# Performance work log

Measured on AMD Instinct MI355X. Metric: run time of the kernel, lower is better.

The kernel has to match this reference:

```python
import jax, jax.numpy as jnp
import numpy as np

CONNECTION_STRENGTH = 3.0   # hardcoded in AMN.forward
DIRECT_WEIGHT = 1.5         # direct_weight_initial
CONN_THRESHOLD = 0.1


def setup_inputs() -> dict:
    key = jax.random.key(0)
    k1, k2, k3, k4, k5 = jax.random.split(key, 5)
    U, T, N = 128, 256, 1024
    return {
        "input_spikes": (jax.random.uniform(k1, (T, N)) < 0.1).astype(jnp.float32),
        "unit_outputs": jax.random.uniform(k2, (U, T, N), dtype=jnp.float32),  # stacked ModularUnit outputs
        "conn": jax.random.uniform(k3, (U, U), dtype=jnp.float32),             # sampled connection matrix
        "target_spikes": (jax.random.uniform(k4, (T, N)) < 0.3).astype(jnp.float32),  # encode_number output
        "rand_bias": jax.random.uniform(k5, (T, N), dtype=jnp.float32),        # torch.rand_like for boost
    }


def reference(input_spikes, unit_outputs, conn, target_spikes, rand_bias):
    # get_spike_rate: mean firing rate in Hz (spikes.mean() * 1000)
    input_rate = input_spikes.mean() * 1000.0
    target_rate = input_rate + 20.0

    # Fused threshold-gated weighted aggregation:
    # for i,j: if conn[i,j] > 0.1: final += unit_outputs[j] * conn[i,j] * 3.0
    gated = jnp.where(conn > CONN_THRESHOLD, conn, 0.0)           # [U,U]
    w = CONNECTION_STRENGTH * gated.sum(axis=0)                   # [U] total inbound weight per source j
    final = jnp.einsum('j,jtn->tn', w, unit_outputs)              # [T,N]

    # Direct mapping heuristic
    final = final * 0.5 + target_spikes * DIRECT_WEIGHT

    # Conditional boost when mean activity is low
    mean = final.mean()
    target_mean = target_rate / 100.0
    boost = jnp.maximum(0.0, target_mean - mean)
    final = jnp.where(mean < 0.2, final + rand_bias * boost * 2.0, final)
    return final
```

## Files before the change

### kernel.cpp

```cpp
#include <hip/hip_runtime.h>

#define U   128
#define T_  256
#define N_  1024
#define TN  (T_ * N_)


__global__ __launch_bounds__(1024) void prep_kernel(const float* __restrict__ conn,
                                                    float* __restrict__ ws) {
    __shared__ float part[8][U];
    int tid = threadIdx.x;
    int c = tid >> 7;
    int j = tid & 127;
    float s = 0.0f;
#pragma unroll
    for (int k = 0; k < 16; ++k) {
        float v = conn[(c * 16 + k) * U + j];
        s += (v > 0.1f) ? v : 0.0f;
    }
    part[c][j] = s;
    __syncthreads();
    if (tid < 2) ws[tid] = 0.0f;
    if (tid < U) {
        float t = 0.0f;
#pragma unroll
        for (int cc = 0; cc < 8; ++cc) t += part[cc][tid];
        ws[2 + tid] = 3.0f * t;
    }
}

__global__ __launch_bounds__(256) void main_kernel(const float* __restrict__ uo,
                                                   const float* __restrict__ tgt,
                                                   const float* __restrict__ insp,
                                                   float* __restrict__ out,
                                                   float* __restrict__ ws) {
    __shared__ float w_s[U];
    int tid = threadIdx.x;
    if (tid < U) w_s[tid] = ws[2 + tid];
    __syncthreads();

    int idx = blockIdx.x * 256 + tid;
    const float* p = uo + idx;

    float acc = 0.0f;
#pragma unroll 16
    for (int j = 0; j < U; ++j)
        acc += w_s[j] * __builtin_nontemporal_load(p + (size_t)j * TN);

    float r = acc * 0.5f + 1.5f * tgt[idx];
    out[idx] = r;
    float lin = insp[idx];

#pragma unroll
    for (int off = 32; off > 0; off >>= 1) {
        r   += __shfl_down(r,   off, 64);
        lin += __shfl_down(lin, off, 64);
    }
    __shared__ float red[8];
    int wave = tid >> 6;
    int lane = tid & 63;
    if (lane == 0) { red[wave] = r; red[4 + wave] = lin; }
    __syncthreads();
    if (tid == 0) {
        atomicAdd(&ws[0], red[0] + red[1] + red[2] + red[3]);
        atomicAdd(&ws[1], red[4] + red[5] + red[6] + red[7]);
    }
}

__global__ __launch_bounds__(256) void boost_kernel(const float4* __restrict__ rb,
                                                    float4* __restrict__ out,
                                                    const float* __restrict__ ws) {
    float mean    = ws[0] * (1.0f / TN);
    float in_rate = ws[1] * (1000.0f / TN);
    float target_mean = (in_rate + 20.0f) * 0.01f;
    float boost = fmaxf(0.0f, target_mean - mean);
    if (mean < 0.2f) {
        int idx = blockIdx.x * 256 + threadIdx.x;
        float4 o = out[idx];
        float4 r = rb[idx];
        float b2 = boost * 2.0f;
        o.x += r.x * b2;
        o.y += r.y * b2;
        o.z += r.z * b2;
        o.w += r.w * b2;
        out[idx] = o;
    }
}

extern "C" void kernel_launch(void* const* d_in, const int* in_sizes, int n_in,
                              void* d_out, int out_size, void* d_ws, size_t ws_size,
                              hipStream_t stream) {
    const float* input_spikes = (const float*)d_in[0];
    const float* unit_outputs = (const float*)d_in[1];
    const float* conn         = (const float*)d_in[2];
    const float* target       = (const float*)d_in[3];
    const float* rand_bias    = (const float*)d_in[4];
    float* out = (float*)d_out;
    float* ws  = (float*)d_ws;

    prep_kernel<<<1, 1024, 0, stream>>>(conn, ws);

    main_kernel<<<TN / 256, 256, 0, stream>>>(
        unit_outputs, target, input_spikes, out, ws);

    boost_kernel<<<(TN / 4) / 256, 256, 0, stream>>>(
        (const float4*)rand_bias, (float4*)out, ws);
}
```

Measured before the change: 214.2 us.

## Split unit reduction across groups with vectorized prefetched loads and combine pass

Splits the 128-unit weighted reduction into 8 groups of 16 units, each handled by separate blocks over 64 tiles. Threads use float4 nontemporal loads with a one-step software prefetch, and write per-group partial sums to workspace. A new combine kernel sums the partials, applies the target term and does the mean reductions. This aims to raise memory-level parallelism and load width on the 128 MB streaming read. In exchange it adds an 8 MB partial-sum write and read-back, plus an extra kernel launch, and it assumes the workspace is large enough.

Result: faster. 204.6 us (-4.4%).

```diff
diff --git a/kernel.cpp b/kernel.cpp
--- a/kernel.cpp
+++ b/kernel.cpp
@@ -1,9 +1,14 @@
 #include <hip/hip_runtime.h>
 
-#define U   128
-#define T_  256
-#define N_  1024
-#define TN  (T_ * N_)
+#define U     128
+#define TN    (256 * 1024)
+#define TN4   (TN / 4)
+#define GJ    8
+#define JPG   (U / GJ)
+#define TILES 64
+#define TILE_F4 (TN4 / TILES)
+
+typedef float vfloat4 __attribute__((ext_vector_type(4)));
 
 
 __global__ __launch_bounds__(1024) void prep_kernel(const float* __restrict__ conn,
@@ -29,46 +34,84 @@
     }
 }
 
-__global__ __launch_bounds__(256) void main_kernel(const float* __restrict__ uo,
-                                                   const float* __restrict__ tgt,
-                                                   const float* __restrict__ insp,
-                                                   float* __restrict__ out,
+__global__ __launch_bounds__(256) void main_kernel(const vfloat4* __restrict__ uo,
                                                    float* __restrict__ ws) {
-    __shared__ float w_s[U];
-    int tid = threadIdx.x;
-    if (tid < U) w_s[tid] = ws[2 + tid];
-    __syncthreads();
+    int tile = blockIdx.x & (TILES - 1);
+    int g    = blockIdx.x / TILES;
+    int tid  = threadIdx.x;
 
-    int idx = blockIdx.x * 256 + tid;
-    const float* p = uo + idx;
+    const float* wp = ws + 2 + g * JPG;
+    vfloat4* part = (vfloat4*)(ws + 256) + (size_t)g * TN4;
 
-    float acc = 0.0f;
-#pragma unroll 16
-    for (int j = 0; j < U; ++j)
-        acc += w_s[j] * __builtin_nontemporal_load(p + (size_t)j * TN);
+    size_t base = (size_t)tile * TILE_F4 + tid;
+    const vfloat4* pu = uo + (size_t)(g * JPG) * TN4 + base;
 
-    float r = acc * 0.5f + 1.5f * tgt[idx];
+    vfloat4 acc0 = 0.0f, acc1 = 0.0f, acc2 = 0.0f, acc3 = 0.0f;
+
+    vfloat4 b0 = __builtin_nontemporal_load(pu + 0);
+    vfloat4 b1 = __builtin_nontemporal_load(pu + 256);
+    vfloat4 b2 = __builtin_nontemporal_load(pu + 512);
+    vfloat4 b3 = __builtin_nontemporal_load(pu + 768);
+
+    for (int jj = 0; jj < JPG; ++jj) {
+        float wj = wp[jj];
+        vfloat4 c0 = b0, c1 = b1, c2 = b2, c3 = b3;
+        if (jj + 1 < JPG) {
+            const vfloat4* pn = pu + (size_t)(jj + 1) * TN4;
+            b0 = __builtin_nontemporal_load(pn + 0);
+            b1 = __builtin_nontemporal_load(pn + 256);
+            b2 = __builtin_nontemporal_load(pn + 512);
+            b3 = __builtin_nontemporal_load(pn + 768);
+        }
+        acc0 += wj * c0;
+        acc1 += wj * c1;
+        acc2 += wj * c2;
+        acc3 += wj * c3;
+    }
+
+    part[base + 0]   = acc0;
+    part[base + 256] = acc1;
+    part[base + 512] = acc2;
+    part[base + 768] = acc3;
+}
+
+__global__ __launch_bounds__(256) void combine_kernel(const vfloat4* __restrict__ tgt,
+                                                      const vfloat4* __restrict__ insp,
+                                                      vfloat4* __restrict__ out,
+                                                      float* __restrict__ ws) {
+    int idx = blockIdx.x * 256 + threadIdx.x;
+    const vfloat4* part = (const vfloat4*)(ws + 256);
+
+    vfloat4 s = part[idx];
+#pragma unroll
+    for (int g = 1; g < GJ; ++g)
+        s += part[(size_t)g * TN4 + idx];
+
+    vfloat4 t = tgt[idx];
+    vfloat4 r = s * 0.5f + 1.5f * t;
     out[idx] = r;
-    float lin = insp[idx];
 
+    vfloat4 is = insp[idx];
+    float lsum = r.x + r.y + r.z + r.w;
+    float lin  = is.x + is.y + is.z + is.w;
 #pragma unroll
     for (int off = 32; off > 0; off >>= 1) {
-        r   += __shfl_down(r,   off, 64);
-        lin += __shfl_down(lin, off, 64);
+        lsum += __shfl_down(lsum, off, 64);
+        lin  += __shfl_down(lin,  off, 64);
     }
     __shared__ float red[8];
-    int wave = tid >> 6;
-    int lane = tid & 63;
-    if (lane == 0) { red[wave] = r; red[4 + wave] = lin; }
+    int wave = threadIdx.x >> 6;
+    int lane = threadIdx.x & 63;
+    if (lane == 0) { red[wave] = lsum; red[4 + wave] = lin; }
     __syncthreads();
-    if (tid == 0) {
+    if (threadIdx.x == 0) {
         atomicAdd(&ws[0], red[0] + red[1] + red[2] + red[3]);
         atomicAdd(&ws[1], red[4] + red[5] + red[6] + red[7]);
     }
 }
 
-__global__ __launch_bounds__(256) void boost_kernel(const float4* __restrict__ rb,
-                                                    float4* __restrict__ out,
+__global__ __launch_bounds__(256) void boost_kernel(const vfloat4* __restrict__ rb,
+                                                    vfloat4* __restrict__ out,
                                                     const float* __restrict__ ws) {
     float mean    = ws[0] * (1.0f / TN);
     float in_rate = ws[1] * (1000.0f / TN);
@@ -76,14 +119,9 @@
     float boost = fmaxf(0.0f, target_mean - mean);
     if (mean < 0.2f) {
         int idx = blockIdx.x * 256 + threadIdx.x;
-        float4 o = out[idx];
-        float4 r = rb[idx];
-        float b2 = boost * 2.0f;
-        o.x += r.x * b2;
-        o.y += r.y * b2;
-        o.z += r.z * b2;
-        o.w += r.w * b2;
-        out[idx] = o;
+        vfloat4 o = out[idx];
+        vfloat4 r = rb[idx];
+        out[idx] = o + r * (boost * 2.0f);
     }
 }
 
@@ -100,9 +138,12 @@
 
     prep_kernel<<<1, 1024, 0, stream>>>(conn, ws);
 
-    main_kernel<<<TN / 256, 256, 0, stream>>>(
-        unit_outputs, target, input_spikes, out, ws);
+    main_kernel<<<TILES * GJ, 256, 0, stream>>>(
+        (const vfloat4*)unit_outputs, ws);
 
-    boost_kernel<<<(TN / 4) / 256, 256, 0, stream>>>(
-        (const float4*)rand_bias, (float4*)out, ws);
+    combine_kernel<<<TN4 / 256, 256, 0, stream>>>(
+        (const vfloat4*)target, (const vfloat4*)input_spikes, (vfloat4*)out, ws);
+
+    boost_kernel<<<TN4 / 256, 256, 0, stream>>>(
+        (const vfloat4*)rand_bias, (vfloat4*)out, ws);
 }
```

## Fuse conn prep into main kernel, vectorize loads, replace atomics with per-block partials

Applied to the files above, without the earlier changes.

The gate-and-sum over conn now runs redundantly in every block of the main kernel, which removes the separate single-block prep launch. The main kernel loads float4 vectors, so it runs only 256 blocks with four outputs per thread. Per-block partial sums go to workspace slots instead of atomics, and the boost kernel reduces these 256 partials in each block before applying the boost. The risk is fewer blocks in flight for a bandwidth-bound 128 MB stream, plus the redundant conn reads per block.

After: 192.8 us. -10.0%, faster.

```diff
diff --git a/kernel.cpp b/kernel.cpp
--- a/kernel.cpp
+++ b/kernel.cpp
@@ -1,89 +1,95 @@
 #include <hip/hip_runtime.h>
 
-#define U   128
-#define T_  256
-#define N_  1024
-#define TN  (T_ * N_)
+#define U    128
+#define TN   (256 * 1024)
+#define TN4  (TN / 4)
+#define NBLK 256
+
+typedef float vfloat4 __attribute__((ext_vector_type(4)));
 
 
-__global__ __launch_bounds__(1024) void prep_kernel(const float* __restrict__ conn,
-                                                    float* __restrict__ ws) {
-    __shared__ float part[8][U];
-    int tid = threadIdx.x;
-    int c = tid >> 7;
-    int j = tid & 127;
-    float s = 0.0f;
-#pragma unroll
-    for (int k = 0; k < 16; ++k) {
-        float v = conn[(c * 16 + k) * U + j];
-        s += (v > 0.1f) ? v : 0.0f;
-    }
-    part[c][j] = s;
-    __syncthreads();
-    if (tid < 2) ws[tid] = 0.0f;
-    if (tid < U) {
-        float t = 0.0f;
-#pragma unroll
-        for (int cc = 0; cc < 8; ++cc) t += part[cc][tid];
-        ws[2 + tid] = 3.0f * t;
-    }
-}
-
-__global__ __launch_bounds__(256) void main_kernel(const float* __restrict__ uo,
-                                                   const float* __restrict__ tgt,
-                                                   const float* __restrict__ insp,
-                                                   float* __restrict__ out,
-                                                   float* __restrict__ ws) {
+__global__ __launch_bounds__(256) void fused_kernel(const float*   __restrict__ conn,
+                                                    const vfloat4* __restrict__ uo,
+                                                    const vfloat4* __restrict__ tgt,
+                                                    const vfloat4* __restrict__ insp,
+                                                    vfloat4*       __restrict__ out,
+                                                    float*         __restrict__ ws) {
+    __shared__ float wpart[2][U];
     __shared__ float w_s[U];
     int tid = threadIdx.x;
-    if (tid < U) w_s[tid] = ws[2 + tid];
+
+    {
+        int j = tid & 127;
+        int h = tid >> 7;
+        const float* cp = conn + (size_t)(h * 64) * U + j;
+        float s = 0.0f;
+#pragma unroll
+        for (int k = 0; k < 64; ++k) {
+            float v = cp[(size_t)k * U];
+            s += (v > 0.1f) ? v : 0.0f;
+        }
+        wpart[h][j] = s;
+    }
+    __syncthreads();
+    if (tid < U) w_s[tid] = 3.0f * (wpart[0][tid] + wpart[1][tid]);
     __syncthreads();
 
     int idx = blockIdx.x * 256 + tid;
-    const float* p = uo + idx;
+    const vfloat4* p = uo + idx;
+    vfloat4 acc = 0.0f;
+#pragma unroll 16
+    for (int jj = 0; jj < U; ++jj)
+        acc += w_s[jj] * __builtin_nontemporal_load(p + (size_t)jj * TN4);
 
-    float acc = 0.0f;
-#pragma unroll 16
-    for (int j = 0; j < U; ++j)
-        acc += w_s[j] * __builtin_nontemporal_load(p + (size_t)j * TN);
+    vfloat4 t = tgt[idx];
+    vfloat4 r = acc * 0.5f + 1.5f * t;
+    out[idx] = r;
 
-    float r = acc * 0.5f + 1.5f * tgt[idx];
-    out[idx] = r;
-    float lin = insp[idx];
-
+    vfloat4 is = insp[idx];
+    float lsum = r.x + r.y + r.z + r.w;
+    float lin  = is.x + is.y + is.z + is.w;
 #pragma unroll
     for (int off = 32; off > 0; off >>= 1) {
-        r   += __shfl_down(r,   off, 64);
-        lin += __shfl_down(lin, off, 64);
+        lsum += __shfl_down(lsum, off, 64);
+        lin  += __shfl_down(lin,  off, 64);
     }
     __shared__ float red[8];
     int wave = tid >> 6;
     int lane = tid & 63;
-    if (lane == 0) { red[wave] = r; red[4 + wave] = lin; }
+    if (lane == 0) { red[wave] = lsum; red[4 + wave] = lin; }
     __syncthreads();
     if (tid == 0) {
-        atomicAdd(&ws[0], red[0] + red[1] + red[2] + red[3]);
-        atomicAdd(&ws[1], red[4] + red[5] + red[6] + red[7]);
+        ws[blockIdx.x]        = red[0] + red[1] + red[2] + red[3];
+        ws[NBLK + blockIdx.x] = red[4] + red[5] + red[6] + red[7];
     }
 }
 
-__global__ __launch_bounds__(256) void boost_kernel(const float4* __restrict__ rb,
-                                                    float4* __restrict__ out,
-                                                    const float* __restrict__ ws) {
-    float mean    = ws[0] * (1.0f / TN);
-    float in_rate = ws[1] * (1000.0f / TN);
+__global__ __launch_bounds__(256) void boost_kernel(const vfloat4* __restrict__ rb,
+                                                    vfloat4*       __restrict__ out,
+                                                    const float*   __restrict__ ws) {
+    int tid = threadIdx.x;
+    float lsum = ws[tid];
+    float lin  = ws[NBLK + tid];
+#pragma unroll
+    for (int off = 32; off > 0; off >>= 1) {
+        lsum += __shfl_down(lsum, off, 64);
+        lin  += __shfl_down(lin,  off, 64);
+    }
+    __shared__ float red[8];
+    int wave = tid >> 6;
+    int lane = tid & 63;
+    if (lane == 0) { red[wave] = lsum; red[4 + wave] = lin; }
+    __syncthreads();
+    float tot = red[0] + red[1] + red[2] + red[3];
+    float tin = red[4] + red[5] + red[6] + red[7];
+
+    float mean        = tot * (1.0f / TN);
+    float in_rate     = tin * (1000.0f / TN);
     float target_mean = (in_rate + 20.0f) * 0.01f;
-    float boost = fmaxf(0.0f, target_mean - mean);
+    float boost       = fmaxf(0.0f, target_mean - mean);
     if (mean < 0.2f) {
-        int idx = blockIdx.x * 256 + threadIdx.x;
-        float4 o = out[idx];
-        float4 r = rb[idx];
-        float b2 = boost * 2.0f;
-        o.x += r.x * b2;
-        o.y += r.y * b2;
-        o.z += r.z * b2;
-        o.w += r.w * b2;
-        out[idx] = o;
+        int idx = blockIdx.x * 256 + tid;
+        out[idx] += rb[idx] * (boost * 2.0f);
     }
 }
 
@@ -98,11 +104,10 @@
     float* out = (float*)d_out;
     float* ws  = (float*)d_ws;
 
-    prep_kernel<<<1, 1024, 0, stream>>>(conn, ws);
+    fused_kernel<<<NBLK, 256, 0, stream>>>(
+        conn, (const vfloat4*)unit_outputs, (const vfloat4*)target,
+        (const vfloat4*)input_spikes, (vfloat4*)out, ws);
 
-    main_kernel<<<TN / 256, 256, 0, stream>>>(
-        unit_outputs, target, input_spikes, out, ws);
-
-    boost_kernel<<<(TN / 4) / 256, 256, 0, stream>>>(
-        (const float4*)rand_bias, (float4*)out, ws);
+    boost_kernel<<<TN4 / 256, 256, 0, stream>>>(
+        (const vfloat4*)rand_bias, (vfloat4*)out, ws);
 }
```
